# Kernel tuning notes

Hardware: AMD Instinct MI355X
Metric: run time of the kernel (lower is better)

## Reference

```python
import jax, jax.numpy as jnp
import numpy as np

HEADS = 16
DIM_HEAD = 64
LN_EPS = 1e-5


def rotate_half(t):
    # '... (j d) -> ... j d' with j=2, then cat(-x2, x1)
    d = t.shape[-1] // 2
    t1, t2 = t[..., :d], t[..., d:]
    return jnp.concatenate([-t2, t1], axis=-1)


def apply_rotary_pos_emb(t, pos):
    # t: (BT, h, L, dh); pos: (L, rotate_dim)
    rd = pos.shape[-1]
    pos = pos[None, None]  # (1, 1, L, rd)
    t_rot, t_pass = t[..., :rd], t[..., rd:]
    t_rot = t_rot * jnp.cos(pos) + rotate_half(t_rot) * jnp.sin(pos)
    return jnp.concatenate([t_rot, t_pass], axis=-1)


def setup_inputs() -> dict:
    key = jax.random.key(0)
    ks = jax.random.split(key, 4)
    B, T, L, D = 2, 8, 1024, 1024
    inner = HEADS * DIM_HEAD
    x = jax.random.normal(ks[0], (B, T * L, D), dtype=jnp.float32)
    gamma = jnp.ones((D,), jnp.float32)
    beta = jnp.zeros((D,), jnp.float32)
    W_qkv = jax.random.normal(ks[1], (D, 3 * inner), jnp.float32) * (D ** -0.5)
    b_qkv = jnp.zeros((3 * inner,), jnp.float32)
    W_out = jax.random.normal(ks[2], (inner, D), jnp.float32) * (inner ** -0.5)
    # standard GPT-NeoX-style rope angles for the spatial axis, rotate_dim=32
    rot_dim = 32
    inv_freq = 1.0 / (10000.0 ** (jnp.arange(0, rot_dim, 2, dtype=jnp.float32) / rot_dim))
    freqs = jnp.arange(L, dtype=jnp.float32)[:, None] * inv_freq[None, :]  # (L, 16)
    rotary_pos_emb = jnp.concatenate([freqs, freqs], axis=-1)  # (L, 32)
    return {"x": x, "gamma": gamma, "beta": beta, "W_qkv": W_qkv,
            "b_qkv": b_qkv, "W_out": W_out, "rotary_pos_emb": rotary_pos_emb,
            "T": T, "L": L}


def reference(x, gamma, beta, W_qkv, b_qkv, W_out, rotary_pos_emb, T, L):
    B, _, D = x.shape
    h, dh = HEADS, DIM_HEAD
    scale = dh ** -0.5
    # LayerNorm
    mean = jnp.mean(x, axis=-1, keepdims=True)
    var = jnp.mean(jnp.square(x - mean), axis=-1, keepdims=True)
    xn = (x - mean) * jax.lax.rsqrt(var + LN_EPS) * gamma + beta
    # (B, T*L, D) -> (B*T, L, D)
    xr = xn.reshape(B * T, L, D)
    qkv = xr @ W_qkv + b_qkv  # (BT, L, 3*h*dh)
    q, k, v = jnp.split(qkv, 3, axis=-1)
    def to_heads(t):
        return t.reshape(B * T, L, h, dh).transpose(0, 2, 1, 3)  # (BT, h, L, dh)
    q, k, v = map(to_heads, (q, k, v))
    q = apply_rotary_pos_emb(q, rotary_pos_emb)
    k = apply_rotary_pos_emb(k, rotary_pos_emb)
    sim = jnp.einsum('bhid,bhjd->bhij', q, k) * scale
    attn = jax.nn.softmax(sim.astype(jnp.float32), axis=-1).astype(q.dtype)
    out = jnp.einsum('bhij,bhjd->bhid', attn, v)  # (BT, h, L, dh)
    out = out.transpose(0, 2, 1, 3).reshape(B * T, L, h * dh)
    out = out @ W_out  # (BT, L, D)
    return out.reshape(B, T * L, D)
```

## Files before the change

kernel.cpp:

```cpp
#include <hip/hip_runtime.h>
#include <hip/hip_bf16.h>
#include <stdint.h>

typedef short bf16x8 __attribute__((ext_vector_type(8)));
typedef float f32x4  __attribute__((ext_vector_type(4)));
typedef unsigned short u16x4 __attribute__((ext_vector_type(4)));
typedef unsigned int   u32x2 __attribute__((ext_vector_type(2)));

#define DEV __device__ __forceinline__

DEV ushort f2bf(float f){
  unsigned u = __float_as_uint(f);
  u += 0x7FFFu + ((u >> 16) & 1u);
  return (ushort)(u >> 16);
}
DEV float bf2f(ushort h){ return __uint_as_float(((unsigned)h) << 16); }

DEV unsigned pack_bf16x2(float lo, float hi){
  __hip_bfloat162 r = __float22bfloat162_rn(float2{lo, hi});
  return *(unsigned*)&r;
}

DEV void async16(const void* g, void* l){
  __builtin_amdgcn_global_load_lds((const __attribute__((address_space(1))) void*)g,
                                   (__attribute__((address_space(3))) void*)l, 16, 0, 0);
}

__global__ __launch_bounds__(256) void ln_kernel(const float* __restrict__ x,
    const float* __restrict__ gamma, const float* __restrict__ beta,
    ushort* __restrict__ xn)
{
  int row = blockIdx.x;
  int t = threadIdx.x;
  const float4* xr = (const float4*)(x + (size_t)row * 1024);
  float4 v = xr[t];
  float s  = v.x + v.y + v.z + v.w;
  float s2 = v.x*v.x + v.y*v.y + v.z*v.z + v.w*v.w;
  #pragma unroll
  for (int o = 1; o < 64; o <<= 1) { s += __shfl_xor(s, o); s2 += __shfl_xor(s2, o); }
  __shared__ float red[8];
  int lane = t & 63, wv = t >> 6;
  if (lane == 0) { red[wv] = s; red[4 + wv] = s2; }
  __syncthreads();
  s  = red[0] + red[1] + red[2] + red[3];
  s2 = red[4] + red[5] + red[6] + red[7];
  float mean = s * (1.0f / 1024.0f);
  float var  = s2 * (1.0f / 1024.0f) - mean * mean;
  float rs = rsqrtf(var + 1e-5f);
  const float4* g4 = (const float4*)gamma;
  const float4* b4 = (const float4*)beta;
  float4 g = g4[t], b = b4[t];
  u16x4 o4;
  o4[0] = f2bf((v.x - mean) * rs * g.x + b.x);
  o4[1] = f2bf((v.y - mean) * rs * g.y + b.y);
  o4[2] = f2bf((v.z - mean) * rs * g.z + b.z);
  o4[3] = f2bf((v.w - mean) * rs * g.w + b.w);
  ((u16x4*)(xn + (size_t)row * 1024))[t] = o4;
}

__global__ __launch_bounds__(256) void trans_f32_bf16(const float* __restrict__ A,
    ushort* __restrict__ At, int R, int C)
{
  __shared__ __align__(16) ushort tile[64][65];
  int c0 = blockIdx.x * 64, r0 = blockIdx.y * 64;
  int tx = threadIdx.x & 63, ty = threadIdx.x >> 6;
  #pragma unroll
  for (int i = 0; i < 64; i += 4)
    tile[ty + i][tx] = f2bf(A[(size_t)(r0 + ty + i) * C + c0 + tx]);
  __syncthreads();
  #pragma unroll
  for (int i = 0; i < 64; i += 4)
    At[(size_t)(c0 + ty + i) * R + r0 + tx] = tile[tx][ty + i];
}

__global__ __launch_bounds__(256) void rope_tab(const float* __restrict__ rope,
    float2* __restrict__ cst)
{
  int i = blockIdx.x * 256 + threadIdx.x;
  int l = i >> 4, d = i & 15;
  float p = rope[l * 32 + d];
  float s, c;
  sincosf(p, &s, &c);
  cst[i] = float2{c, s};
}

template<bool OUT_BF16, bool HAS_BIAS, bool ROPE>
__global__ __launch_bounds__(512, 2) void gemm256_kernel(
    const ushort* __restrict__ A, const ushort* __restrict__ Bt,
    const float* __restrict__ bias, void* __restrict__ Cout,
    const float2* __restrict__ cst,
    int M, int Nrow, int K, int nbx, int colbase)
{
  __shared__ __align__(16) ushort As[2][2][256][32];
  __shared__ __align__(16) ushort Bs[2][2][256][32];
  const int tid = threadIdx.x, lane = tid & 63, w = tid >> 6;
  const int fr = lane & 15, fg = lane >> 4;
  const int wr = w >> 2, wc = w & 3;

  int nwg = gridDim.x, cpx = nwg >> 3;
  int logical = (blockIdx.x & 7) * cpx + (blockIdx.x >> 3);
  int bx = logical % nbx, by = logical / nbx;
  const int aRow0 = by * 256, bCol0 = bx * 256;
  const size_t ldb = (size_t)K * 2;

  const int lrow = lane >> 2, lch = lane & 3;
  const int g0 = w * 2, g1 = w * 2 + 1;
  const int r0 = g0 * 16 + lrow, r1 = g1 * 16 + lrow;
  const int sc0 = ((lch ^ ((r0 & 3) ^ ((r0 >> 2) & 3))) << 4);
  const int sc1 = ((lch ^ ((r1 & 3) ^ ((r1 >> 2) & 3))) << 4);
  const char* Ab = (const char*)A + (size_t)aRow0 * ldb;
  const char* Bb = (const char*)Bt + (size_t)bCol0 * ldb;
  const size_t ga0 = (size_t)r0 * ldb, ga1 = (size_t)r1 * ldb;
  char* ldsA = (char*)&As[0][0][0][0];
  char* ldsB = (char*)&Bs[0][0][0][0];
  const int ld0 = g0 * 1024, ld1 = g1 * 1024;

  int rbA[8], rbB[4];
  #pragma unroll
  for (int mf = 0; mf < 8; ++mf) {
    int rr = wr * 128 + mf * 16 + fr;
    rbA[mf] = rr * 64 + ((fg ^ ((rr & 3) ^ ((rr >> 2) & 3))) << 4);
  }
  #pragma unroll
  for (int nf = 0; nf < 4; ++nf) {
    int rr = wc * 64 + nf * 16 + fr;
    rbB[nf] = rr * 64 + ((fg ^ ((rr & 3) ^ ((rr >> 2) & 3))) << 4);
  }

  f32x4 acc[8][4];
  f32x4 z = {0.f, 0.f, 0.f, 0.f};
  #pragma unroll
  for (int mf = 0; mf < 8; ++mf)
    #pragma unroll
    for (int nf = 0; nf < 4; ++nf) acc[mf][nf] = z;

  auto stage = [&](int buf, int kt, int kc) {
    const char* ak = Ab + (size_t)kt * 128 + kc * 64;
    const char* bk = Bb + (size_t)kt * 128 + kc * 64;
    int lo = buf * 32768 + kc * 16384;
    async16(ak + ga0 + sc0, ldsA + lo + ld0);
    async16(ak + ga1 + sc1, ldsA + lo + ld1);
    async16(bk + ga0 + sc0, ldsB + lo + ld0);
    async16(bk + ga1 + sc1, ldsB + lo + ld1);
  };

  stage(0, 0, 0);
  stage(0, 0, 1);
  asm volatile("s_waitcnt vmcnt(4)" ::: "memory");
  __builtin_amdgcn_s_barrier();

  const int nk = K >> 6;
  for (int kt = 0; kt < nk; ++kt) {
    int buf = kt & 1;
    bool pre = (kt + 1 < nk);
    #pragma unroll
    for (int kc = 0; kc < 2; ++kc) {
      const char* ab = ldsA + buf * 32768 + kc * 16384;
      const char* bb = ldsB + buf * 32768 + kc * 16384;
      bf16x8 a[8], b[4];
      #pragma unroll
      for (int mf = 0; mf < 8; ++mf) a[mf] = *(const bf16x8*)(ab + rbA[mf]);
      #pragma unroll
      for (int nf = 0; nf < 4; ++nf) b[nf] = *(const bf16x8*)(bb + rbB[nf]);
      if (pre) stage(buf ^ 1, kt + 1, kc);
      __builtin_amdgcn_s_setprio(1);
      #pragma unroll
      for (int mf = 0; mf < 8; ++mf)
        #pragma unroll
        for (int nf = 0; nf < 4; ++nf)
          acc[mf][nf] = __builtin_amdgcn_mfma_f32_16x16x32_bf16(a[mf], b[nf], acc[mf][nf], 0, 0, 0);
      __builtin_amdgcn_s_setprio(0);
      if (pre) { asm volatile("s_waitcnt vmcnt(4)" ::: "memory"); }
      else     { asm volatile("s_waitcnt vmcnt(0)" ::: "memory"); }
      __builtin_amdgcn_s_barrier();
    }
  }

  #pragma unroll
  for (int pr = 0; pr < 2; ++pr) {
    int nf0 = pr * 2, nf1 = nf0 + 1;
    int gc0 = colbase + bCol0 + wc * 64 + nf0 * 16 + fr;
    int gc1 = gc0 + 16;
    float bv0 = HAS_BIAS ? bias[gc0] : 0.0f;
    float bv1 = HAS_BIAS ? bias[gc1] : 0.0f;
    bool rot = ROPE && (pr == 0) && (gc0 < 2048);
    float qs = (ROPE && gc0 < 1024) ? 0.18033688f : 1.0f;
    #pragma unroll
    for (int mf = 0; mf < 8; ++mf) {
      int gr0 = aRow0 + wr * 128 + mf * 16 + fg * 4;
      #pragma unroll
      for (int r = 0; r < 4; ++r) {
        int gr = gr0 + r;
        float a = acc[mf][nf0][r] + bv0;
        float b = acc[mf][nf1][r] + bv1;
        if (rot) {
          int l = gr & 1023;
          float2 cp = cst[l * 16 + fr];
          float an = fmaf(a, cp.x, -b * cp.y);
          b = fmaf(b, cp.x, a * cp.y);
          a = an;
        }
        a *= qs; b *= qs;
        if (OUT_BF16) {
          ((ushort*)Cout)[(size_t)gr * Nrow + gc0] = f2bf(a);
          ((ushort*)Cout)[(size_t)gr * Nrow + gc1] = f2bf(b);
        } else {
          ((float*)Cout)[(size_t)gr * Nrow + gc0] = a;
          ((float*)Cout)[(size_t)gr * Nrow + gc1] = b;
        }
      }
    }
  }
}

__global__ __launch_bounds__(256) void vtrans_kernel(const ushort* __restrict__ qkv,
                                                     ushort* __restrict__ vT)
{
  __shared__ __align__(16) ushort tile[64][65];
  int bh = blockIdx.x & 255, lt = blockIdx.x >> 8;
  int bt = bh >> 4, h = bh & 15;
  int tx = threadIdx.x & 63, ty = threadIdx.x >> 6;
  const ushort* src = qkv + (size_t)(bt * 1024 + lt * 64) * 3072 + 2048 + h * 64;
  #pragma unroll
  for (int i = 0; i < 64; i += 4)
    tile[ty + i][tx] = src[(size_t)(ty + i) * 3072 + tx];
  __syncthreads();
  ushort* dst = vT + (size_t)bh * 64 * 1024 + lt * 64;
  #pragma unroll
  for (int i = 0; i < 64; i += 4)
    dst[(size_t)(ty + i) * 1024 + tx] = tile[tx][ty + i];
}

__global__ __launch_bounds__(256, 3) void attn_kernel(
    const ushort* __restrict__ qkv, const ushort* __restrict__ vT,
    ushort* __restrict__ aout)
{
  __shared__ __align__(16) ushort Ks[2][64 * 64];
  __shared__ __align__(16) ushort Vs[2][64 * 64];
  __shared__ __align__(16) ushort Ps[4][32 * 64];
  const int tid = threadIdx.x, lane = tid & 63, w = tid >> 6;
  const int fr = lane & 15, fg = lane >> 4;
  const int bh = blockIdx.x & 255, qt = blockIdx.x >> 8;
  const int bt = bh >> 4, h = bh & 15;
  const size_t ld = 3072;
  const ushort* qbase = qkv + (size_t)bt * 1024 * ld + h * 64;
  const ushort* kbase = qbase + 1024;
  const ushort* vtb = vT + (size_t)bh * 64 * 1024;
  const int srow = lane >> 3;
  const int scol = (((lane & 7) ^ srow) << 4);
  const int swz = (fr & 7) << 4;

  bf16x8 ones;
  #pragma unroll
  for (int j = 0; j < 8; ++j) ones[j] = (short)0x3F80;

  bf16x8 qfr[2][2];
  #pragma unroll
  for (int qf = 0; qf < 2; ++qf)
    #pragma unroll
    for (int kc = 0; kc < 2; ++kc) {
      int qrow = qt * 128 + w * 32 + qf * 16 + fr;
      qfr[qf][kc] = *(const bf16x8*)((const char*)(qbase + (size_t)qrow * ld) + kc * 64 + fg * 16);
    }

  f32x4 o[2][4], ls[2];
  f32x4 z = {0.f, 0.f, 0.f, 0.f};
  #pragma unroll
  for (int a = 0; a < 2; ++a) {
    ls[a] = z;
    #pragma unroll
    for (int b = 0; b < 4; ++b) o[a][b] = z;
  }
  float m_[2] = {-1e30f, -1e30f};

  auto stage = [&](int buf, int t) {
    #pragma unroll
    for (int i = 0; i < 2; ++i) {
      int ch = w * 2 + i;
      async16((const char*)(kbase + (size_t)(t * 64 + ch * 8 + srow) * ld) + scol,
              (char*)Ks[buf] + ch * 1024);
      async16((const char*)(vtb + (size_t)(ch * 8 + srow) * 1024) + t * 128 + scol,
              (char*)Vs[buf] + ch * 1024);
    }
  };

  stage(0, 0);
  __syncthreads();
  for (int t = 0; t < 16; ++t) {
    int cur = t & 1;
    if (t + 1 < 16) stage(cur ^ 1, t + 1);

    bf16x8 kf[4][2];
    #pragma unroll
    for (int kvf = 0; kvf < 4; ++kvf)
      #pragma unroll
      for (int kc = 0; kc < 2; ++kc)
        kf[kvf][kc] = *(const bf16x8*)((const char*)Ks[cur] + (kvf * 16 + fr) * 128 +
                                       ((kc * 64 + fg * 16) ^ swz));
    float alpha[2] = {1.0f, 1.0f};
    int   need[2];
    #pragma unroll
    for (int qf = 0; qf < 2; ++qf) {
      f32x4 st[4];
      #pragma unroll
      for (int kvf = 0; kvf < 4; ++kvf) st[kvf] = z;
      __builtin_amdgcn_s_setprio(1);
      #pragma unroll
      for (int kc = 0; kc < 2; ++kc)
        #pragma unroll
        for (int kvf = 0; kvf < 4; ++kvf)
          st[kvf] = __builtin_amdgcn_mfma_f32_16x16x32_bf16(kf[kvf][kc], qfr[qf][kc], st[kvf], 0, 0, 0);
      __builtin_amdgcn_s_setprio(0);
      float mx = -1e30f;
      #pragma unroll
      for (int kvf = 0; kvf < 4; ++kvf)
        #pragma unroll
        for (int r = 0; r < 4; ++r) mx = fmaxf(mx, st[kvf][r]);
      mx = fmaxf(mx, __shfl_xor(mx, 16));
      mx = fmaxf(mx, __shfl_xor(mx, 32));
      need[qf] = __any(mx > m_[qf] + 11.53f);
      if (need[qf]) {
        float mn = fmaxf(m_[qf], mx);
        alpha[qf] = __builtin_amdgcn_exp2f(m_[qf] - mn);
        m_[qf] = mn;
      }
      float mb = m_[qf];
      int qrow = qf * 16 + fr;
      #pragma unroll
      for (int kvf = 0; kvf < 4; ++kvf) {
        float p0 = __builtin_amdgcn_exp2f(st[kvf][0] - mb);
        float p1 = __builtin_amdgcn_exp2f(st[kvf][1] - mb);
        float p2 = __builtin_amdgcn_exp2f(st[kvf][2] - mb);
        float p3 = __builtin_amdgcn_exp2f(st[kvf][3] - mb);
        u32x2 u;
        u[0] = pack_bf16x2(p0, p1);
        u[1] = pack_bf16x2(p2, p3);
        *(u32x2*)((char*)Ps[w] + qrow * 128 + ((kvf * 32 + fg * 8) ^ swz)) = u;
      }
    }
    #pragma unroll
    for (int of = 0; of < 2; ++of) {
      if (need[of]) {
        float ar[4];
        #pragma unroll
        for (int r = 0; r < 4; ++r) ar[r] = __shfl(alpha[of], fg * 4 + r);
        #pragma unroll
        for (int cf = 0; cf < 4; ++cf)
          #pragma unroll
          for (int r = 0; r < 4; ++r) o[of][cf][r] *= ar[r];
        #pragma unroll
        for (int r = 0; r < 4; ++r) ls[of][r] *= ar[r];
      }
    }
    __builtin_amdgcn_s_setprio(1);
    #pragma unroll
    for (int kc4 = 0; kc4 < 2; ++kc4) {
      bf16x8 pa[2];
      #pragma unroll
      for (int of = 0; of < 2; ++of)
        pa[of] = *(const bf16x8*)((const char*)Ps[w] + (of * 16 + fr) * 128 +
                                  ((kc4 * 64 + fg * 16) ^ swz));
      #pragma unroll
      for (int cf = 0; cf < 4; ++cf) {
        bf16x8 vb = *(const bf16x8*)((const char*)Vs[cur] + (cf * 16 + fr) * 128 +
                                     ((kc4 * 64 + fg * 16) ^ swz));
        #pragma unroll
        for (int of = 0; of < 2; ++of)
          o[of][cf] = __builtin_amdgcn_mfma_f32_16x16x32_bf16(pa[of], vb, o[of][cf], 0, 0, 0);
      }
      #pragma unroll
      for (int of = 0; of < 2; ++of)
        ls[of] = __builtin_amdgcn_mfma_f32_16x16x32_bf16(pa[of], ones, ls[of], 0, 0, 0);
    }
    __builtin_amdgcn_s_setprio(0);
    __syncthreads();
  }
  #pragma unroll
  for (int of = 0; of < 2; ++of) {
    #pragma unroll
    for (int cf = 0; cf < 4; ++cf)
      #pragma unroll
      for (int r = 0; r < 4; ++r) {
        int grow_ = bt * 1024 + qt * 128 + w * 32 + of * 16 + fg * 4 + r;
        int gcol  = h * 64 + cf * 16 + fr;
        aout[(size_t)grow_ * 1024 + gcol] = f2bf(o[of][cf][r] / ls[of][r]);
      }
  }
}

extern "C" void kernel_launch(void* const* d_in, const int* in_sizes, int n_in,
                              void* d_out, int out_size, void* d_ws, size_t ws_size,
                              hipStream_t stream)
{
  const float* x     = (const float*)d_in[0];
  const float* gamma = (const float*)d_in[1];
  const float* beta  = (const float*)d_in[2];
  const float* Wqkv  = (const float*)d_in[3];
  const float* bqkv  = (const float*)d_in[4];
  const float* Wout  = (const float*)d_in[5];
  const float* rope  = (const float*)d_in[6];

  char* ws = (char*)d_ws;
  ushort* xn   = (ushort*)(ws + 0);
  ushort* qkvb = (ushort*)(ws + 33554432ULL);
  ushort* vT   = (ushort*)(ws + 134217728ULL);
  ushort* Wqt  = (ushort*)(ws + 167772160ULL);
  ushort* Wot  = (ushort*)(ws + 174063616ULL);
  float2* cst  = (float2*)(ws + 176160768ULL);
  ushort* aout = xn;

  ln_kernel<<<16384, 256, 0, stream>>>(x, gamma, beta, xn);
  trans_f32_bf16<<<dim3(48, 16), 256, 0, stream>>>(Wqkv, Wqt, 1024, 3072);
  trans_f32_bf16<<<dim3(16, 16), 256, 0, stream>>>(Wout, Wot, 1024, 1024);
  rope_tab<<<64, 256, 0, stream>>>(rope, cst);
  for (int seg = 0; seg < 3; ++seg) {
    gemm256_kernel<true, true, true><<<256, 512, 0, stream>>>(
        xn, Wqt + (size_t)seg * 1024 * 1024, bqkv, (void*)qkvb,
        cst, 16384, 3072, 1024, 4, seg * 1024);
  }
  vtrans_kernel<<<4096, 256, 0, stream>>>(qkvb, vT);
  attn_kernel<<<2048, 256, 0, stream>>>(qkvb, vT, aout);
  gemm256_kernel<false, false, false><<<256, 512, 0, stream>>>(
      aout, Wot, nullptr, d_out, nullptr, 16384, 1024, 1024, 4, 0);
}
```

Before: 327.0 us.

## Merge preprocessing kernels, launch QKV GEMM once, double attention block size

After: 323.3 us. No clear change (-1.1%).

```diff
diff --git a/kernel.cpp b/kernel.cpp
--- a/kernel.cpp
+++ b/kernel.cpp
@@ -14,7 +14,6 @@
   u += 0x7FFFu + ((u >> 16) & 1u);
   return (ushort)(u >> 16);
 }
-DEV float bf2f(ushort h){ return __uint_as_float(((unsigned)h) << 16); }
 
 DEV unsigned pack_bf16x2(float lo, float hi){
   __hip_bfloat162 r = __float22bfloat162_rn(float2{lo, hi});
@@ -26,62 +25,60 @@
                                    (__attribute__((address_space(3))) void*)l, 16, 0, 0);
 }
 
-__global__ __launch_bounds__(256) void ln_kernel(const float* __restrict__ x,
-    const float* __restrict__ gamma, const float* __restrict__ beta,
-    ushort* __restrict__ xn)
-{
-  int row = blockIdx.x;
-  int t = threadIdx.x;
-  const float4* xr = (const float4*)(x + (size_t)row * 1024);
-  float4 v = xr[t];
-  float s  = v.x + v.y + v.z + v.w;
-  float s2 = v.x*v.x + v.y*v.y + v.z*v.z + v.w*v.w;
-  #pragma unroll
-  for (int o = 1; o < 64; o <<= 1) { s += __shfl_xor(s, o); s2 += __shfl_xor(s2, o); }
-  __shared__ float red[8];
-  int lane = t & 63, wv = t >> 6;
-  if (lane == 0) { red[wv] = s; red[4 + wv] = s2; }
-  __syncthreads();
-  s  = red[0] + red[1] + red[2] + red[3];
-  s2 = red[4] + red[5] + red[6] + red[7];
-  float mean = s * (1.0f / 1024.0f);
-  float var  = s2 * (1.0f / 1024.0f) - mean * mean;
-  float rs = rsqrtf(var + 1e-5f);
-  const float4* g4 = (const float4*)gamma;
-  const float4* b4 = (const float4*)beta;
-  float4 g = g4[t], b = b4[t];
-  u16x4 o4;
-  o4[0] = f2bf((v.x - mean) * rs * g.x + b.x);
-  o4[1] = f2bf((v.y - mean) * rs * g.y + b.y);
-  o4[2] = f2bf((v.z - mean) * rs * g.z + b.z);
-  o4[3] = f2bf((v.w - mean) * rs * g.w + b.w);
-  ((u16x4*)(xn + (size_t)row * 1024))[t] = o4;
-}
-
-__global__ __launch_bounds__(256) void trans_f32_bf16(const float* __restrict__ A,
-    ushort* __restrict__ At, int R, int C)
+__global__ __launch_bounds__(256) void preproc_kernel(
+    const float* __restrict__ x, const float* __restrict__ gamma,
+    const float* __restrict__ beta, ushort* __restrict__ xn,
+    const float* __restrict__ Wqkv, ushort* __restrict__ Wqt,
+    const float* __restrict__ Wout, ushort* __restrict__ Wot,
+    const float* __restrict__ rope, float2* __restrict__ cst)
 {
   __shared__ __align__(16) ushort tile[64][65];
-  int c0 = blockIdx.x * 64, r0 = blockIdx.y * 64;
-  int tx = threadIdx.x & 63, ty = threadIdx.x >> 6;
-  #pragma unroll
-  for (int i = 0; i < 64; i += 4)
-    tile[ty + i][tx] = f2bf(A[(size_t)(r0 + ty + i) * C + c0 + tx]);
-  __syncthreads();
-  #pragma unroll
-  for (int i = 0; i < 64; i += 4)
-    At[(size_t)(c0 + ty + i) * R + r0 + tx] = tile[tx][ty + i];
-}
-
-__global__ __launch_bounds__(256) void rope_tab(const float* __restrict__ rope,
-    float2* __restrict__ cst)
-{
-  int i = blockIdx.x * 256 + threadIdx.x;
-  int l = i >> 4, d = i & 15;
-  float p = rope[l * 32 + d];
-  float s, c;
-  sincosf(p, &s, &c);
-  cst[i] = float2{c, s};
+  __shared__ float red[8];
+  const int b = blockIdx.x, t = threadIdx.x;
+  if (b < 16384) {
+    const float4* xr = (const float4*)(x + (size_t)b * 1024);
+    float4 v = xr[t];
+    float s  = v.x + v.y + v.z + v.w;
+    float s2 = v.x*v.x + v.y*v.y + v.z*v.z + v.w*v.w;
+    #pragma unroll
+    for (int o = 1; o < 64; o <<= 1) { s += __shfl_xor(s, o); s2 += __shfl_xor(s2, o); }
+    int lane = t & 63, wv = t >> 6;
+    if (lane == 0) { red[wv] = s; red[4 + wv] = s2; }
+    __syncthreads();
+    s  = red[0] + red[1] + red[2] + red[3];
+    s2 = red[4] + red[5] + red[6] + red[7];
+    float mean = s * (1.0f / 1024.0f);
+    float var  = s2 * (1.0f / 1024.0f) - mean * mean;
+    float rs = rsqrtf(var + 1e-5f);
+    float4 g = ((const float4*)gamma)[t], bb = ((const float4*)beta)[t];
+    u16x4 o4;
+    o4[0] = f2bf((v.x - mean) * rs * g.x + bb.x);
+    o4[1] = f2bf((v.y - mean) * rs * g.y + bb.y);
+    o4[2] = f2bf((v.z - mean) * rs * g.z + bb.z);
+    o4[3] = f2bf((v.w - mean) * rs * g.w + bb.w);
+    ((u16x4*)(xn + (size_t)b * 1024))[t] = o4;
+  } else if (b < 17408) {
+    const float* A; ushort* At; int R, C, c0, r0;
+    if (b < 17152) { int bb2 = b - 16384; A = Wqkv; At = Wqt; R = 1024; C = 3072;
+                     c0 = (bb2 % 48) * 64; r0 = (bb2 / 48) * 64; }
+    else           { int bb2 = b - 17152; A = Wout; At = Wot; R = 1024; C = 1024;
+                     c0 = (bb2 % 16) * 64; r0 = (bb2 / 16) * 64; }
+    int tx = t & 63, ty = t >> 6;
+    #pragma unroll
+    for (int i = 0; i < 64; i += 4)
+      tile[ty + i][tx] = f2bf(A[(size_t)(r0 + ty + i) * C + c0 + tx]);
+    __syncthreads();
+    #pragma unroll
+    for (int i = 0; i < 64; i += 4)
+      At[(size_t)(c0 + ty + i) * R + r0 + tx] = tile[tx][ty + i];
+  } else {
+    int i = (b - 17408) * 256 + t;
+    int l = i >> 4, d = i & 15;
+    float p = rope[l * 32 + d];
+    float s, c;
+    sincosf(p, &s, &c);
+    cst[i] = float2{c, s};
+  }
 }
 
 template<bool OUT_BF16, bool HAS_BIAS, bool ROPE>
@@ -89,7 +86,7 @@
     const ushort* __restrict__ A, const ushort* __restrict__ Bt,
     const float* __restrict__ bias, void* __restrict__ Cout,
     const float2* __restrict__ cst,
-    int M, int Nrow, int K, int nbx, int colbase)
+    int M, int Nrow, int K)
 {
   __shared__ __align__(16) ushort As[2][2][256][32];
   __shared__ __align__(16) ushort Bs[2][2][256][32];
@@ -97,9 +94,11 @@
   const int fr = lane & 15, fg = lane >> 4;
   const int wr = w >> 2, wc = w & 3;
 
-  int nwg = gridDim.x, cpx = nwg >> 3;
-  int logical = (blockIdx.x & 7) * cpx + (blockIdx.x >> 3);
-  int bx = logical % nbx, by = logical / nbx;
+  int i  = blockIdx.x & 255;
+  int r  = blockIdx.x >> 8;
+  int il = (i & 7) * 32 + (i >> 3);
+  int bx = r * 4 + (il & 3);
+  int by = il >> 2;
   const int aRow0 = by * 256, bCol0 = bx * 256;
   const size_t ldb = (size_t)K * 2;
 
@@ -179,7 +178,7 @@
   #pragma unroll
   for (int pr = 0; pr < 2; ++pr) {
     int nf0 = pr * 2, nf1 = nf0 + 1;
-    int gc0 = colbase + bCol0 + wc * 64 + nf0 * 16 + fr;
+    int gc0 = bCol0 + wc * 64 + nf0 * 16 + fr;
     int gc1 = gc0 + 16;
     float bv0 = HAS_BIAS ? bias[gc0] : 0.0f;
     float bv1 = HAS_BIAS ? bias[gc1] : 0.0f;
@@ -189,10 +188,10 @@
     for (int mf = 0; mf < 8; ++mf) {
       int gr0 = aRow0 + wr * 128 + mf * 16 + fg * 4;
       #pragma unroll
-      for (int r = 0; r < 4; ++r) {
-        int gr = gr0 + r;
-        float a = acc[mf][nf0][r] + bv0;
-        float b = acc[mf][nf1][r] + bv1;
+      for (int rr2 = 0; rr2 < 4; ++rr2) {
+        int gr = gr0 + rr2;
+        float a = acc[mf][nf0][rr2] + bv0;
+        float b = acc[mf][nf1][rr2] + bv1;
         if (rot) {
           int l = gr & 1023;
           float2 cp = cst[l * 16 + fr];
@@ -231,13 +230,13 @@
     dst[(size_t)(ty + i) * 1024 + tx] = tile[tx][ty + i];
 }
 
-__global__ __launch_bounds__(256, 3) void attn_kernel(
+__global__ __launch_bounds__(512, 4) void attn_kernel(
     const ushort* __restrict__ qkv, const ushort* __restrict__ vT,
     ushort* __restrict__ aout)
 {
   __shared__ __align__(16) ushort Ks[2][64 * 64];
   __shared__ __align__(16) ushort Vs[2][64 * 64];
-  __shared__ __align__(16) ushort Ps[4][32 * 64];
+  __shared__ __align__(16) ushort Ps[8][32 * 64];
   const int tid = threadIdx.x, lane = tid & 63, w = tid >> 6;
   const int fr = lane & 15, fg = lane >> 4;
   const int bh = blockIdx.x & 255, qt = blockIdx.x >> 8;
@@ -259,7 +258,7 @@
   for (int qf = 0; qf < 2; ++qf)
     #pragma unroll
     for (int kc = 0; kc < 2; ++kc) {
-      int qrow = qt * 128 + w * 32 + qf * 16 + fr;
+      int qrow = qt * 256 + w * 32 + qf * 16 + fr;
       qfr[qf][kc] = *(const bf16x8*)((const char*)(qbase + (size_t)qrow * ld) + kc * 64 + fg * 16);
     }
 
@@ -274,14 +273,10 @@
   float m_[2] = {-1e30f, -1e30f};
 
   auto stage = [&](int buf, int t) {
-    #pragma unroll
-    for (int i = 0; i < 2; ++i) {
-      int ch = w * 2 + i;
-      async16((const char*)(kbase + (size_t)(t * 64 + ch * 8 + srow) * ld) + scol,
-              (char*)Ks[buf] + ch * 1024);
-      async16((const char*)(vtb + (size_t)(ch * 8 + srow) * 1024) + t * 128 + scol,
-              (char*)Vs[buf] + ch * 1024);
-    }
+    async16((const char*)(kbase + (size_t)(t * 64 + w * 8 + srow) * ld) + scol,
+            (char*)Ks[buf] + w * 1024);
+    async16((const char*)(vtb + (size_t)(w * 8 + srow) * 1024) + t * 128 + scol,
+            (char*)Vs[buf] + w * 1024);
   };
 
   stage(0, 0);
@@ -381,7 +376,7 @@
     for (int cf = 0; cf < 4; ++cf)
       #pragma unroll
       for (int r = 0; r < 4; ++r) {
-        int grow_ = bt * 1024 + qt * 128 + w * 32 + of * 16 + fg * 4 + r;
+        int grow_ = bt * 1024 + qt * 256 + w * 32 + of * 16 + fg * 4 + r;
         int gcol  = h * 64 + cf * 16 + fr;
         aout[(size_t)grow_ * 1024 + gcol] = f2bf(o[of][cf][r] / ls[of][r]);
       }
@@ -409,17 +404,12 @@
   float2* cst  = (float2*)(ws + 176160768ULL);
   ushort* aout = xn;
 
-  ln_kernel<<<16384, 256, 0, stream>>>(x, gamma, beta, xn);
-  trans_f32_bf16<<<dim3(48, 16), 256, 0, stream>>>(Wqkv, Wqt, 1024, 3072);
-  trans_f32_bf16<<<dim3(16, 16), 256, 0, stream>>>(Wout, Wot, 1024, 1024);
-  rope_tab<<<64, 256, 0, stream>>>(rope, cst);
-  for (int seg = 0; seg < 3; ++seg) {
-    gemm256_kernel<true, true, true><<<256, 512, 0, stream>>>(
-        xn, Wqt + (size_t)seg * 1024 * 1024, bqkv, (void*)qkvb,
-        cst, 16384, 3072, 1024, 4, seg * 1024);
-  }
+  preproc_kernel<<<17472, 256, 0, stream>>>(x, gamma, beta, xn,
+                                            Wqkv, Wqt, Wout, Wot, rope, cst);
+  gemm256_kernel<true, true, true><<<768, 512, 0, stream>>>(
+      xn, Wqt, bqkv, (void*)qkvb, cst, 16384, 3072, 1024);
   vtrans_kernel<<<4096, 256, 0, stream>>>(qkvb, vT);
-  attn_kernel<<<2048, 256, 0, stream>>>(qkvb, vT, aout);
+  attn_kernel<<<1024, 512, 0, stream>>>(qkvb, vT, aout);
   gemm256_kernel<false, false, false><<<256, 512, 0, stream>>>(
-      aout, Wot, nullptr, d_out, nullptr, 16384, 1024, 1024, 4, 0);
-}
+      aout, Wot, nullptr, d_out, nullptr, 16384, 1024, 1024);
+}
```
